# Kernel optimization log

Measured on AMD Instinct MI355X. Metric: run time of the kernel, lower is better.

The kernel has to match this reference:

```python
import jax, jax.numpy as jnp
import numpy as np

EMBED_DIM = 1024
N_HEADS = 16

def setup_inputs() -> dict:
    key = jax.random.key(0)
    k1, k2, k3 = jax.random.split(key, 3)
    x = jax.random.normal(k1, (4, 2048, EMBED_DIM), dtype=jnp.float32)
    # nn.Linear(D, 3D): store weight as [D, 3D] for x @ W
    W_qkv = jax.random.normal(k2, (EMBED_DIM, 3 * EMBED_DIM), dtype=jnp.float32) * (1.0 / np.sqrt(EMBED_DIM))
    b_qkv = jax.random.normal(k3, (3 * EMBED_DIM,), dtype=jnp.float32) * 0.02
    return {"x": x, "W_qkv": W_qkv, "b_qkv": b_qkv}

def reference(x, W_qkv, b_qkv):
    bs, T, D = x.shape
    nh = N_HEADS
    hs = D // nh
    # fused qkv projection -> [bs, T, nh, 3, hs] (matches view(bs,T,nh,3*hs) + split(hs))
    qkv = (jnp.einsum('btd,de->bte', x, W_qkv) + b_qkv).reshape(bs, T, nh, 3, hs)
    q = qkv[..., 0, :].transpose(0, 2, 1, 3)  # [bs, nh, T, hs]
    k = qkv[..., 1, :].transpose(0, 2, 1, 3)
    v = qkv[..., 2, :].transpose(0, 2, 1, 3)
    scale = 1.0 / np.sqrt(hs).astype(np.float32)
    scores = jnp.einsum('bhqd,bhkd->bhqk', q, k) * scale  # [bs, nh, T, T]
    attn = jax.nn.softmax(scores, axis=-1)
    out = jnp.einsum('bhqk,bhkd->bhqd', attn, v)  # [bs, nh, T, hs]
    return out.transpose(0, 2, 1, 3).reshape(bs, T, D)
```

## Files before the change

### kernel.cpp

```cpp
#include <hip/hip_runtime.h>
#include <stdint.h>

#define T_SEQ 2048
#define DMODEL 1024
#define NHEAD 16
#define HS 64
#define N3 3072
#define BSZ 4
#define MTOT (BSZ*T_SEQ)

typedef __attribute__((ext_vector_type(8))) short bf16x8;
typedef __attribute__((ext_vector_type(4))) float f32x4;
typedef __attribute__((ext_vector_type(16))) float f32x16;
typedef __attribute__((ext_vector_type(2))) unsigned int uint2v;

#define QSCALE 0.18033688011112042f
#define SM_SHIFT 12.0f

#define BH_STRIDE 131072

__device__ inline unsigned short f2bf(float f){
  union { float f; uint32_t u; } v; v.f = f;
  uint32_t r = (v.u + 0x7fffu + ((v.u >> 16) & 1u)) >> 16;
  return (unsigned short)r;
}

__device__ inline uint32_t cvtpk_bf16(float lo, float hi){
  uint32_t r;
  asm("v_cvt_pk_bf16_f32 %0, %1, %2" : "=v"(r) : "v"(lo), "v"(hi));
  return r;
}

__device__ inline void plswap(uint32_t &a, uint32_t &b){
  uint2v r = __builtin_amdgcn_permlane32_swap(a, b, false, false);
  a = r[0]; b = r[1];
}

__device__ inline void gld16(const void* g, void* l){
  __builtin_amdgcn_global_load_lds((const __attribute__((address_space(1))) void*)g,
                                   (__attribute__((address_space(3))) void*)l, 16, 0, 0);
}

__global__ __launch_bounds__(256) void cvt_x(const float* __restrict__ x,
                                             unsigned short* __restrict__ xb, int n){
  int stride = gridDim.x * blockDim.x;
  for (int i = blockIdx.x * blockDim.x + threadIdx.x; i * 4 < n; i += stride){
    const float4 v = *(const float4*)(x + (size_t)i * 4);
    ushort4 o; o.x = f2bf(v.x); o.y = f2bf(v.y); o.z = f2bf(v.z); o.w = f2bf(v.w);
    *(ushort4*)(xb + (size_t)i * 4) = o;
  }
}

__global__ __launch_bounds__(256) void cvt_wt(const float* __restrict__ W,
                                              unsigned short* __restrict__ Wt){
  __shared__ float tile[32][33];
  int bx = blockIdx.x;
  int by = blockIdx.y;
  int tx = threadIdx.x;
  int ty = threadIdx.y;
#pragma unroll
  for (int i = 0; i < 4; i++){
    int k = by * 32 + ty + i * 8;
    int n = bx * 32 + tx;
    tile[ty + i * 8][tx] = W[(size_t)k * N3 + n];
  }
  __syncthreads();
#pragma unroll
  for (int i = 0; i < 4; i++){
    int n = bx * 32 + ty + i * 8;
    int k = by * 32 + tx;
    Wt[(size_t)n * DMODEL + k] = f2bf(tile[tx][ty + i * 8]);
  }
}

#define BM 128
#define BN 128
#define BK 32

__global__ __launch_bounds__(256, 2) void gemm_qkv(
    const unsigned short* __restrict__ xb, const unsigned short* __restrict__ wt,
    const float* __restrict__ bias,
    unsigned short* __restrict__ Qb, unsigned short* __restrict__ Kb,
    unsigned short* __restrict__ Vt)
{
  __shared__ unsigned short Al[BM * BK];
  __shared__ unsigned short Bl[BN * BK];
  const int tid = threadIdx.x;
  const int lane = tid & 63;
  const int w  = tid >> 6;
  const int wm = w >> 1, wn = w & 1;
  const int lr = lane & 15, lg = lane >> 4;
  const int m0 = blockIdx.x * BM;
  const int n0 = blockIdx.y * BN;

  f32x4 acc[4][4] = {};

  const int srow = tid >> 2;
  const int scol = ((tid & 3) ^ ((srow >> 1) & 3)) * 8;
  const unsigned short* ga0 = xb + (size_t)(m0 + srow) * DMODEL + scol;
  const unsigned short* gb0 = wt + (size_t)(n0 + srow) * DMODEL + scol;
  unsigned short* la = &Al[tid * 8];
  unsigned short* lb = &Bl[tid * 8];

  const int lgp = lg ^ ((lr >> 1) & 3);

  for (int k0 = 0; k0 < DMODEL; k0 += BK){
    gld16(ga0 + k0, la);
    gld16(ga0 + k0 + (size_t)64 * DMODEL, la + 2048);
    gld16(gb0 + k0, lb);
    gld16(gb0 + k0 + (size_t)64 * DMODEL, lb + 2048);
    __syncthreads();
    bf16x8 af[4], bfg[4];
#pragma unroll
    for (int i = 0; i < 4; i++){
      af[i]  = *(const bf16x8*)&Al[(wm * 64 + i * 16 + lr) * BK + lgp * 8];
      bfg[i] = *(const bf16x8*)&Bl[(wn * 64 + i * 16 + lr) * BK + lgp * 8];
    }
#pragma unroll
    for (int i = 0; i < 4; i++)
#pragma unroll
      for (int j = 0; j < 4; j++)
        acc[i][j] = __builtin_amdgcn_mfma_f32_16x16x32_bf16(af[i], bfg[j], acc[i][j], 0, 0, 0);
    __syncthreads();
  }

#pragma unroll
  for (int i = 0; i < 4; i++){
#pragma unroll
    for (int j = 0; j < 4; j++){
      int gn = n0 + wn * 64 + j * 16 + lr;
      float bv = bias[gn];
      int h = gn / 192;
      int rem = gn - h * 192;
      int which = rem >> 6;
      int d = rem & 63;
#pragma unroll
      for (int r = 0; r < 4; r++){
        int gm = m0 + wm * 64 + i * 16 + lg * 4 + r;
        int b = gm >> 11, t = gm & 2047;
        float val = acc[i][j][r] + bv;
        size_t base = (size_t)(b * NHEAD + h) * BH_STRIDE + (size_t)(t >> 5) * 2048;
        if (which == 0)
          Qb[base + (d >> 4) * 512 + ((d >> 3) & 1) * 256 + (t & 31) * 8 + (d & 7)] = f2bf(val * QSCALE);
        else if (which == 1)
          Kb[base + (d >> 4) * 512 + ((d >> 3) & 1) * 256 + (t & 31) * 8 + (d & 7)] = f2bf(val);
        else {
          int kv = t & 31;
          Vt[base + (d >> 5) * 1024 + (kv >> 4) * 512 + ((kv >> 3) & 1) * 256 + (d & 31) * 8 + (kv & 7)] = f2bf(val);
        }
      }
    }
  }
}

__global__ __launch_bounds__(256, 3) void attn(
    const unsigned short* __restrict__ Qb, const unsigned short* __restrict__ Kb,
    const unsigned short* __restrict__ Vt, float* __restrict__ out)
{
  __shared__ unsigned short KVs[2][2][2][2048];

  int flat = blockIdx.x + (blockIdx.y << 4) + (blockIdx.z << 8);
  int wid = (flat & 7) * 128 + (flat >> 3);
  const int bx = wid & 15;
  const int h  = (wid >> 4) & 15;
  const int b  = wid >> 8;

  const int tid = threadIdx.x;
  const int lane = tid & 63;
  const int w = tid >> 6;
  const int ql = lane & 31;
  const int hi = lane >> 5;
  const int bh = b * NHEAD + h;
  const int q0 = bx * 128 + w * 32;

  const unsigned short* Qf = Qb + (size_t)bh * BH_STRIDE;
  const unsigned short* Kg = Kb + (size_t)bh * BH_STRIDE;
  const unsigned short* Vg = Vt + (size_t)bh * BH_STRIDE;

  bf16x8 qf[4];
#pragma unroll
  for (int c = 0; c < 4; c++)
    qf[c] = *(const bf16x8*)(Qf + (size_t)(q0 >> 5) * 2048 + c * 512 + lane * 8);

  f32x16 cinit;
#pragma unroll
  for (int r = 0; r < 16; r++) cinit[r] = -SM_SHIFT;

  f32x16 acc0 = {}, acc1 = {};
  float lA = 0.f, lB = 0.f, lC = 0.f, lD = 0.f;

  gld16(Kg +        tid * 8, &KVs[0][0][0][tid * 8]);
  gld16(Kg + 2048 + tid * 8, &KVs[0][0][1][tid * 8]);
  gld16(Vg +        tid * 8, &KVs[0][1][0][tid * 8]);
  gld16(Vg + 2048 + tid * 8, &KVs[0][1][1][tid * 8]);
  __syncthreads();

#define SOFTMAX_PACK(S, PF1, PF2) \
    uint32_t c8[8]; \
    _Pragma("unroll") \
    for (int i = 0; i < 8; i += 2){ \
      float p0 = __builtin_amdgcn_exp2f((S)[2 * i]); \
      float p1 = __builtin_amdgcn_exp2f((S)[2 * i + 1]); \
      float p2 = __builtin_amdgcn_exp2f((S)[2 * i + 2]); \
      float p3 = __builtin_amdgcn_exp2f((S)[2 * i + 3]); \
      lA += p0; lB += p1; lC += p2; lD += p3; \
      c8[i]     = cvtpk_bf16(p0, p1); \
      c8[i + 1] = cvtpk_bf16(p2, p3); \
    } \
    plswap(c8[0], c8[2]); plswap(c8[1], c8[3]); \
    plswap(c8[4], c8[6]); plswap(c8[5], c8[7]); \
    PF1.u[0] = c8[0]; PF1.u[1] = c8[1]; PF1.u[2] = c8[2]; PF1.u[3] = c8[3]; \
    PF2.u[0] = c8[4]; PF2.u[1] = c8[5]; PF2.u[2] = c8[6]; PF2.u[3] = c8[7];

  for (int t = 0; t < 32; ++t){
    const int cur = t & 1;
    if (t < 31){
      const size_t g0 = (size_t)(2 * t + 2) * 2048 + tid * 8;
      gld16(Kg + g0,        &KVs[cur ^ 1][0][0][tid * 8]);
      gld16(Kg + g0 + 2048, &KVs[cur ^ 1][0][1][tid * 8]);
      gld16(Vg + g0,        &KVs[cur ^ 1][1][0][tid * 8]);
      gld16(Vg + g0 + 2048, &KVs[cur ^ 1][1][1][tid * 8]);
    }

    f32x16 sA;
    {
      bf16x8 kf[4];
#pragma unroll
      for (int c = 0; c < 4; c++) kf[c] = *(const bf16x8*)&KVs[cur][0][0][c * 512 + lane * 8];
      __builtin_amdgcn_s_setprio(1);
      sA = __builtin_amdgcn_mfma_f32_32x32x16_bf16(kf[0], qf[0], cinit, 0, 0, 0);
      sA = __builtin_amdgcn_mfma_f32_32x32x16_bf16(kf[1], qf[1], sA, 0, 0, 0);
      sA = __builtin_amdgcn_mfma_f32_32x32x16_bf16(kf[2], qf[2], sA, 0, 0, 0);
      sA = __builtin_amdgcn_mfma_f32_32x32x16_bf16(kf[3], qf[3], sA, 0, 0, 0);
      __builtin_amdgcn_s_setprio(0);
    }
    f32x16 sB;
    {
      bf16x8 kf[4];
#pragma unroll
      for (int c = 0; c < 4; c++) kf[c] = *(const bf16x8*)&KVs[cur][0][1][c * 512 + lane * 8];
      __builtin_amdgcn_s_setprio(1);
      sB = __builtin_amdgcn_mfma_f32_32x32x16_bf16(kf[0], qf[0], cinit, 0, 0, 0);
      sB = __builtin_amdgcn_mfma_f32_32x32x16_bf16(kf[1], qf[1], sB, 0, 0, 0);
      sB = __builtin_amdgcn_mfma_f32_32x32x16_bf16(kf[2], qf[2], sB, 0, 0, 0);
      sB = __builtin_amdgcn_mfma_f32_32x32x16_bf16(kf[3], qf[3], sB, 0, 0, 0);
      __builtin_amdgcn_s_setprio(0);
    }

    {
      union { uint32_t u[4]; bf16x8 v; } pf1, pf2;
      SOFTMAX_PACK(sA, pf1, pf2)
      bf16x8 vf[4];
#pragma unroll
      for (int c = 0; c < 4; c++) vf[c] = *(const bf16x8*)&KVs[cur][1][0][c * 512 + lane * 8];
      __builtin_amdgcn_s_setprio(1);
      acc0 = __builtin_amdgcn_mfma_f32_32x32x16_bf16(vf[0], pf1.v, acc0, 0, 0, 0);
      acc0 = __builtin_amdgcn_mfma_f32_32x32x16_bf16(vf[1], pf2.v, acc0, 0, 0, 0);
      acc1 = __builtin_amdgcn_mfma_f32_32x32x16_bf16(vf[2], pf1.v, acc1, 0, 0, 0);
      acc1 = __builtin_amdgcn_mfma_f32_32x32x16_bf16(vf[3], pf2.v, acc1, 0, 0, 0);
      __builtin_amdgcn_s_setprio(0);
    }
    {
      union { uint32_t u[4]; bf16x8 v; } pf1, pf2;
      SOFTMAX_PACK(sB, pf1, pf2)
      bf16x8 vf[4];
#pragma unroll
      for (int c = 0; c < 4; c++) vf[c] = *(const bf16x8*)&KVs[cur][1][1][c * 512 + lane * 8];
      __builtin_amdgcn_s_setprio(1);
      acc0 = __builtin_amdgcn_mfma_f32_32x32x16_bf16(vf[0], pf1.v, acc0, 0, 0, 0);
      acc0 = __builtin_amdgcn_mfma_f32_32x32x16_bf16(vf[1], pf2.v, acc0, 0, 0, 0);
      acc1 = __builtin_amdgcn_mfma_f32_32x32x16_bf16(vf[2], pf1.v, acc1, 0, 0, 0);
      acc1 = __builtin_amdgcn_mfma_f32_32x32x16_bf16(vf[3], pf2.v, acc1, 0, 0, 0);
      __builtin_amdgcn_s_setprio(0);
    }

    __syncthreads();
  }
#undef SOFTMAX_PACK

  float l_ = (lA + lB) + (lC + lD);
  l_ += __shfl_xor(l_, 32);
  float inv = 1.0f / l_;

  float* tl = (float*)&KVs[0][0][0][0];
  float* tw = tl + w * (32 * 33);
#pragma unroll
  for (int t2 = 0; t2 < 2; t2++){
    const f32x16& A = t2 ? acc1 : acc0;
#pragma unroll
    for (int r = 0; r < 16; r++){
      int dp = (r & 3) + 8 * (r >> 2) + 4 * hi;
      tw[dp * 33 + ql] = A[r] * inv;
    }
    asm volatile("s_waitcnt lgkmcnt(0)" ::: "memory");
    const int cq = lane >> 3;
    const int cc = (lane & 7) * 4;
#pragma unroll
    for (int it = 0; it < 4; it++){
      int q = it * 8 + cq;
      float4 o;
      o.x = tw[(cc + 0) * 33 + q];
      o.y = tw[(cc + 1) * 33 + q];
      o.z = tw[(cc + 2) * 33 + q];
      o.w = tw[(cc + 3) * 33 + q];
      *(float4*)(out + ((size_t)(b * T_SEQ + q0 + q)) * DMODEL + h * HS + t2 * 32 + cc) = o;
    }
    asm volatile("s_waitcnt lgkmcnt(0)" ::: "memory");
  }
}

extern "C" void kernel_launch(void* const* d_in, const int* in_sizes, int n_in,
                              void* d_out, int out_size, void* d_ws, size_t ws_size,
                              hipStream_t stream) {
  const float* x  = (const float*)d_in[0];
  const float* Wq = (const float*)d_in[1];
  const float* bq = (const float*)d_in[2];
  float* out = (float*)d_out;
  uint8_t* ws = (uint8_t*)d_ws;

  unsigned short* xb = (unsigned short*)(ws);
  unsigned short* wt = (unsigned short*)(ws + (size_t)16 * 1024 * 1024);
  unsigned short* Qb = (unsigned short*)(ws + (size_t)22 * 1024 * 1024);
  unsigned short* Kb = (unsigned short*)(ws + (size_t)38 * 1024 * 1024);
  unsigned short* Vt = (unsigned short*)(ws + (size_t)54 * 1024 * 1024);

  cvt_x<<<2048, 256, 0, stream>>>(x, xb, MTOT * DMODEL);
  cvt_wt<<<dim3(N3 / 32, DMODEL / 32), dim3(32, 8), 0, stream>>>(Wq, wt);
  gemm_qkv<<<dim3(MTOT / BM, N3 / BN), 256, 0, stream>>>(xb, wt, bq, Qb, Kb, Vt);
  attn<<<dim3(T_SEQ / 128, NHEAD, BSZ), 256, 0, stream>>>(Qb, Kb, Vt, out);
}
```

Baseline: 169.0 us.

## Pre-swizzle weights into MFMA fragment order and double-buffer QKV GEMM loads

The weight conversion kernel now writes W directly in per-lane MFMA fragment order, so the GEMM can load B fragments straight from global memory into registers instead of staging them through LDS. The A tile is double-buffered in LDS, and the next k-step is prefetched while the current one computes. This leaves one barrier per step, and s_setprio is raised around the MFMA block. The new conversion kernel reads W with strided, poorly coalesced accesses, and register pressure rises from holding two sets of B fragments.

```diff
diff --git a/kernel.cpp b/kernel.cpp
--- a/kernel.cpp
+++ b/kernel.cpp
@@ -51,25 +51,26 @@
   }
 }
 
-__global__ __launch_bounds__(256) void cvt_wt(const float* __restrict__ W,
-                                              unsigned short* __restrict__ Wt){
-  __shared__ float tile[32][33];
-  int bx = blockIdx.x;
-  int by = blockIdx.y;
-  int tx = threadIdx.x;
-  int ty = threadIdx.y;
-#pragma unroll
-  for (int i = 0; i < 4; i++){
-    int k = by * 32 + ty + i * 8;
-    int n = bx * 32 + tx;
-    tile[ty + i * 8][tx] = W[(size_t)k * N3 + n];
-  }
-  __syncthreads();
-#pragma unroll
-  for (int i = 0; i < 4; i++){
-    int n = bx * 32 + ty + i * 8;
-    int k = by * 32 + tx;
-    Wt[(size_t)n * DMODEL + k] = f2bf(tile[tx][ty + i * 8]);
+__global__ __launch_bounds__(256) void cvt_wtf(const float* __restrict__ W,
+                                               unsigned short* __restrict__ wtf){
+  const int nt = blockIdx.x;
+  const int ks = blockIdx.y;
+  const int tid = threadIdx.x;
+  const int lr = tid & 15;
+  const int lg = (tid >> 4) & 3;
+  const int fh = tid >> 6;
+#pragma unroll
+  for (int f2 = 0; f2 < 2; f2++){
+    const int f = f2 * 4 + fh;
+    const int wn = f >> 2, j = f & 3;
+    const int n = nt * 128 + wn * 64 + j * 16 + lr;
+    union { unsigned short s[8]; bf16x8 v; } o;
+#pragma unroll
+    for (int e = 0; e < 8; e++){
+      const int k = ks * 32 + lg * 8 + e;
+      o.s[e] = f2bf(W[(size_t)k * N3 + n]);
+    }
+    *(bf16x8*)&wtf[((size_t)(nt * 32 + ks) * 8 + f) * 512 + (tid & 63) * 8] = o.v;
   }
 }
 
@@ -78,13 +79,12 @@
 #define BK 32
 
 __global__ __launch_bounds__(256, 2) void gemm_qkv(
-    const unsigned short* __restrict__ xb, const unsigned short* __restrict__ wt,
+    const unsigned short* __restrict__ xb, const unsigned short* __restrict__ wtf,
     const float* __restrict__ bias,
     unsigned short* __restrict__ Qb, unsigned short* __restrict__ Kb,
     unsigned short* __restrict__ Vt)
 {
-  __shared__ unsigned short Al[BM * BK];
-  __shared__ unsigned short Bl[BN * BK];
+  __shared__ unsigned short Al[2][BM * BK];
   const int tid = threadIdx.x;
   const int lane = tid & 63;
   const int w  = tid >> 6;
@@ -92,37 +92,52 @@
   const int lr = lane & 15, lg = lane >> 4;
   const int m0 = blockIdx.x * BM;
   const int n0 = blockIdx.y * BN;
+  const int nt = blockIdx.y;
 
   f32x4 acc[4][4] = {};
 
   const int srow = tid >> 2;
   const int scol = ((tid & 3) ^ ((srow >> 1) & 3)) * 8;
   const unsigned short* ga0 = xb + (size_t)(m0 + srow) * DMODEL + scol;
-  const unsigned short* gb0 = wt + (size_t)(n0 + srow) * DMODEL + scol;
-  unsigned short* la = &Al[tid * 8];
-  unsigned short* lb = &Bl[tid * 8];
-
   const int lgp = lg ^ ((lr >> 1) & 3);
 
-  for (int k0 = 0; k0 < DMODEL; k0 += BK){
-    gld16(ga0 + k0, la);
-    gld16(ga0 + k0 + (size_t)64 * DMODEL, la + 2048);
-    gld16(gb0 + k0, lb);
-    gld16(gb0 + k0 + (size_t)64 * DMODEL, lb + 2048);
-    __syncthreads();
-    bf16x8 af[4], bfg[4];
-#pragma unroll
-    for (int i = 0; i < 4; i++){
-      af[i]  = *(const bf16x8*)&Al[(wm * 64 + i * 16 + lr) * BK + lgp * 8];
-      bfg[i] = *(const bf16x8*)&Bl[(wn * 64 + i * 16 + lr) * BK + lgp * 8];
-    }
-#pragma unroll
-    for (int i = 0; i < 4; i++)
-#pragma unroll
-      for (int j = 0; j < 4; j++)
-        acc[i][j] = __builtin_amdgcn_mfma_f32_16x16x32_bf16(af[i], bfg[j], acc[i][j], 0, 0, 0);
-    __syncthreads();
-  }
+  const unsigned short* wb = wtf + (size_t)nt * 131072 + wn * 2048 + lane * 8;
+
+  gld16(ga0,                       &Al[0][tid * 8]);
+  gld16(ga0 + (size_t)64 * DMODEL, &Al[0][tid * 8 + 2048]);
+  bf16x8 bfA[4], bfB[4];
+#pragma unroll
+  for (int j = 0; j < 4; j++) bfA[j] = *(const bf16x8*)(wb + j * 512);
+  __syncthreads();
+
+#define GSTEP(KS, CUR, BFC, BFN) { \
+    if ((KS) < 31){ \
+      gld16(ga0 + ((KS) + 1) * 32,                       &Al[(CUR) ^ 1][tid * 8]); \
+      gld16(ga0 + ((KS) + 1) * 32 + (size_t)64 * DMODEL, &Al[(CUR) ^ 1][tid * 8 + 2048]); \
+    } \
+    const int ksn_ = ((KS) + 1 < 32) ? (KS) + 1 : 31; \
+    BFN[0] = *(const bf16x8*)(wb + ksn_ * 4096); \
+    BFN[1] = *(const bf16x8*)(wb + ksn_ * 4096 + 512); \
+    BFN[2] = *(const bf16x8*)(wb + ksn_ * 4096 + 1024); \
+    BFN[3] = *(const bf16x8*)(wb + ksn_ * 4096 + 1536); \
+    bf16x8 af[4]; \
+    _Pragma("unroll") \
+    for (int i = 0; i < 4; i++) \
+      af[i] = *(const bf16x8*)&Al[CUR][(wm * 64 + i * 16 + lr) * BK + lgp * 8]; \
+    __builtin_amdgcn_s_setprio(1); \
+    _Pragma("unroll") \
+    for (int i = 0; i < 4; i++) \
+      _Pragma("unroll") \
+      for (int j = 0; j < 4; j++) \
+        acc[i][j] = __builtin_amdgcn_mfma_f32_16x16x32_bf16(af[i], BFC[j], acc[i][j], 0, 0, 0); \
+    __builtin_amdgcn_s_setprio(0); \
+    __syncthreads(); }
+
+  for (int ks = 0; ks < 32; ks += 2){
+    GSTEP(ks,     0, bfA, bfB)
+    GSTEP(ks + 1, 1, bfB, bfA)
+  }
+#undef GSTEP
 
 #pragma unroll
   for (int i = 0; i < 4; i++){
@@ -318,14 +333,14 @@
   float* out = (float*)d_out;
   uint8_t* ws = (uint8_t*)d_ws;
 
-  unsigned short* xb = (unsigned short*)(ws);
-  unsigned short* wt = (unsigned short*)(ws + (size_t)16 * 1024 * 1024);
-  unsigned short* Qb = (unsigned short*)(ws + (size_t)22 * 1024 * 1024);
-  unsigned short* Kb = (unsigned short*)(ws + (size_t)38 * 1024 * 1024);
-  unsigned short* Vt = (unsigned short*)(ws + (size_t)54 * 1024 * 1024);
+  unsigned short* xb  = (unsigned short*)(ws);
+  unsigned short* wtf = (unsigned short*)(ws + (size_t)16 * 1024 * 1024);
+  unsigned short* Qb  = (unsigned short*)(ws + (size_t)22 * 1024 * 1024);
+  unsigned short* Kb  = (unsigned short*)(ws + (size_t)38 * 1024 * 1024);
+  unsigned short* Vt  = (unsigned short*)(ws + (size_t)54 * 1024 * 1024);
 
   cvt_x<<<2048, 256, 0, stream>>>(x, xb, MTOT * DMODEL);
-  cvt_wt<<<dim3(N3 / 32, DMODEL / 32), dim3(32, 8), 0, stream>>>(Wq, wt);
-  gemm_qkv<<<dim3(MTOT / BM, N3 / BN), 256, 0, stream>>>(xb, wt, bq, Qb, Kb, Vt);
+  cvt_wtf<<<dim3(N3 / 128, 32), 256, 0, stream>>>(Wq, wtf);
+  gemm_qkv<<<dim3(MTOT / BM, N3 / BN), 256, 0, stream>>>(xb, wtf, bq, Qb, Kb, Vt);
   attn<<<dim3(T_SEQ / 128, NHEAD, BSZ), 256, 0, stream>>>(Qb, Kb, Vt, out);
 }
```

New measurement: 160.9 us, median of 2. -4.8%, faster.
